# Kernel optimization log

Hardware: AMD Instinct MI355X
Metric: run time of the kernel (lower is better)

## Reference

```python
import jax, jax.numpy as jnp
import numpy as np

N = 100000   # num_nodes_total
E = 1600000  # num edges (avg degree 16)
ES = 30000   # scored triples
R = 16       # num_relations
D = 128      # cfg.dim


def setup_inputs() -> dict:
    key = jax.random.key(0)
    ks = jax.random.split(key, 10)
    x0 = 0.01 * jax.random.normal(ks[0], (N, D), dtype=jnp.float32)  # Embedding init std=0.01
    # GCNConv lin: Glorot init, no bias in lin; separate zero bias added post-aggregation
    glorot = np.sqrt(6.0 / (D + D)).astype(np.float32)
    W1 = jax.random.uniform(ks[1], (D, D), jnp.float32, -glorot, glorot)
    b1 = jnp.zeros((D,), jnp.float32)
    W2 = jax.random.uniform(ks[2], (D, D), jnp.float32, -glorot, glorot)
    b2 = jnp.zeros((D,), jnp.float32)
    rel_W = jax.random.uniform(ks[3], (R, D, D), jnp.float32, -glorot, glorot)  # xavier_uniform
    edge_index = jax.random.randint(ks[4], (2, E), 0, N)
    rel_ids = jax.random.randint(ks[5], (ES,), 0, R)
    head = jax.random.randint(ks[6], (ES,), 0, N)
    tail = jax.random.randint(ks[7], (ES,), 0, N)
    return {"x0": x0, "W1": W1, "b1": b1, "W2": W2, "b2": b2,
            "rel_W": rel_W, "edge_index": edge_index, "rel_ids": rel_ids,
            "head": head, "tail": tail}


def _gcn_conv(x, W, b, src, dst, norm):
    # GCNConv(add_self_loops=False, normalize=True): out = scatter(norm * (xW)[src] -> dst) + b
    h = x @ W                           # (N, D)
    msg = h[src] * norm[:, None]        # (E, D)
    return jax.ops.segment_sum(msg, dst, num_segments=x.shape[0]) + b


def reference(x0, W1, b1, W2, b2, rel_W, edge_index, rel_ids, head, tail):
    src, dst = edge_index[0], edge_index[1]
    n = x0.shape[0]
    # symmetric gcn_norm without self-loops: deg over targets, norm = d^-1/2[src]*d^-1/2[dst]
    deg = jax.ops.segment_sum(jnp.ones_like(src, dtype=x0.dtype), dst, num_segments=n)
    dinv = jnp.where(deg > 0, 1.0 / jnp.sqrt(jnp.maximum(deg, 1.0)), 0.0)
    norm = dinv[src] * dinv[dst]
    # encode (eval mode: dropout is identity)
    x = jax.nn.relu(_gcn_conv(x0, W1, b1, src, dst, norm))
    z = _gcn_conv(x, W2, b2, src, dst, norm)
    # score_logits_all_rel: z[head]^T W[rel] z[tail]
    scores = jnp.einsum('ed,edf,ef->e', z[head], rel_W[rel_ids], z[tail])
    return scores
```

## Files before the change

### kernel.cpp

```cpp
#include <hip/hip_runtime.h>
#include <hip/hip_bf16.h>

#define TD 128
#define WS 136
#define SC_T 8
#define BKT_SH 7
#define NBLK 256

typedef __attribute__((ext_vector_type(8))) short bf16x8;
typedef __attribute__((ext_vector_type(4))) float f32x4;

static __device__ __forceinline__ unsigned short f2bf(float f) {
    unsigned int u = __float_as_uint(f);
    u += 0x7fffu + ((u >> 16) & 1u);
    return (unsigned short)(u >> 16);
}
static __device__ __forceinline__ float bf2f(unsigned short h) {
    return __uint_as_float((unsigned int)h << 16);
}


__global__ __launch_bounds__(256) void kc_hist(const int* __restrict__ ei, int* __restrict__ bh,
                                               const int* __restrict__ rel, int* __restrict__ rcount,
                                               int E_, int ES_, int NB, int chunk, int rchunk) {
    __shared__ int lh[1024];
    __shared__ int rh[16];
    int t = threadIdx.x, blk = blockIdx.x;
    for (int j = t; j < NB; j += 256) lh[j] = 0;
    if (t < 16) rh[t] = 0;
    __syncthreads();
    int e0 = blk * chunk, e1 = min(E_, e0 + chunk);
    for (int e = e0 + t; e < e1; e += 256)
        atomicAdd(&lh[ei[E_ + e] >> BKT_SH], 1);
    int r0 = blk * rchunk, r1 = min(ES_, r0 + rchunk);
    for (int e = r0 + t; e < r1; e += 256)
        atomicAdd(&rh[rel[e]], 1);
    __syncthreads();
    for (int j = t; j < NB; j += 256) bh[(size_t)j * NBLK + blk] = lh[j];
    if (t < 16 && rh[t]) atomicAdd(&rcount[t], rh[t]);
}

__global__ __launch_bounds__(64) void kc_scanA(int* __restrict__ bh, int* __restrict__ tot, int NB) {
    int b = blockIdx.x, l = threadIdx.x;
    int* row = bh + (size_t)b * NBLK;
    int run = 0;
#pragma unroll
    for (int g = 0; g < NBLK / 64; ++g) {
        int v = row[g * 64 + l];
        int x = v;
#pragma unroll
        for (int off = 1; off < 64; off <<= 1) {
            int y = __shfl_up(x, off);
            if (l >= off) x += y;
        }
        row[g * 64 + l] = run + x - v;
        run += __shfl(x, 63);
    }
    if (l == 0) tot[b] = run;
}

__global__ __launch_bounds__(256) void kc_scanB(const int* __restrict__ tot, int* __restrict__ boff,
                                                int NB, int* __restrict__ rowptrN) {
    __shared__ int wsum[4];
    int t = threadIdx.x;
    int base = t * 4;
    int a0 = (base     < NB) ? tot[base]     : 0;
    int a1 = (base + 1 < NB) ? tot[base + 1] : 0;
    int a2 = (base + 2 < NB) ? tot[base + 2] : 0;
    int a3 = (base + 3 < NB) ? tot[base + 3] : 0;
    int s1 = a0 + a1, s2 = s1 + a2, tt = s2 + a3;
    int lane = t & 63, wv = t >> 6;
    int x = tt;
#pragma unroll
    for (int off = 1; off < 64; off <<= 1) {
        int y = __shfl_up(x, off);
        if (lane >= off) x += y;
    }
    if (lane == 63) wsum[wv] = x;
    __syncthreads();
    int woff = 0;
    for (int w = 0; w < wv; ++w) woff += wsum[w];
    int excl = woff + x - tt;
    if (base     < NB) boff[base]     = excl;
    if (base + 1 < NB) boff[base + 1] = excl + a0;
    if (base + 2 < NB) boff[base + 2] = excl + s1;
    if (base + 3 < NB) boff[base + 3] = excl + s2;
    if (t == 255) { boff[NB] = woff + x; *rowptrN = woff + x; }
}

__global__ __launch_bounds__(256) void kc_scat(const int* __restrict__ ei, const int* __restrict__ bh,
                                               const int* __restrict__ boff, int* __restrict__ ebuf,
                                               int E_, int NB, int chunk) {
    __shared__ int lh[1024];
    int t = threadIdx.x, blk = blockIdx.x;
    for (int j = t; j < NB; j += 256) lh[j] = 0;
    __syncthreads();
    int e0 = blk * chunk, e1 = min(E_, e0 + chunk);
    for (int e = e0 + t; e < e1; e += 256) {
        int s = ei[e];
        int d = ei[E_ + e];
        int b = d >> BKT_SH;
        int lr = atomicAdd(&lh[b], 1);
        int slot = boff[b] + bh[(size_t)b * NBLK + blk] + lr;
        ebuf[slot] = (s << BKT_SH) | (d & ((1 << BKT_SH) - 1));
    }
}

__global__ __launch_bounds__(256) void kc_build(const int* __restrict__ ebuf, const int* __restrict__ boff,
                                                int* __restrict__ rowptr, float* __restrict__ dinv,
                                                int* __restrict__ esrc, int n) {
    __shared__ int hist[128], excl[128], cur[128];
    __shared__ int w0;
    int b = blockIdx.x, t = threadIdx.x;
    int node0 = b << BKT_SH;
    int s = boff[b], e = boff[b + 1];
    if (t < 128) { hist[t] = 0; cur[t] = 0; }
    __syncthreads();
    for (int i = s + t; i < e; i += 256)
        atomicAdd(&hist[ebuf[i] & 127], 1);
    __syncthreads();
    int v = (t < 128) ? hist[t] : 0;
    int lane = t & 63, wv = t >> 6;
    int x = v;
#pragma unroll
    for (int off = 1; off < 64; off <<= 1) {
        int y = __shfl_up(x, off);
        if (lane >= off) x += y;
    }
    if (t == 63) w0 = x;
    __syncthreads();
    if (t < 128) {
        int ex = x - v + (wv == 1 ? w0 : 0);
        excl[t] = ex;
        int node = node0 + t;
        if (node < n) {
            rowptr[node] = s + ex;
            dinv[node] = (v > 0) ? 1.0f / sqrtf((float)v) : 0.0f;
        }
    }
    __syncthreads();
    for (int i = s + t; i < e; i += 256) {
        int p = ebuf[i];
        int loc = p & 127;
        int lr = atomicAdd(&cur[loc], 1);
        esrc[s + excl[loc] + lr] = p >> BKT_SH;
    }
}

__global__ __launch_bounds__(256) void k_wsplit(const float* __restrict__ W1, const float* __restrict__ W2,
                                                unsigned short* __restrict__ Wt) {
    int i = blockIdx.x * 256 + threadIdx.x;
    int w = i >> 14;
    int idx = i & 16383;
    int k = idx >> 7, n = idx & 127;
    float x = (w ? W2 : W1)[idx];
    unsigned short h = f2bf(x);
    unsigned short l = f2bf(x - bf2f(h));
    size_t base = (size_t)w * 32768;
    Wt[base + n * 128 + k] = h;
    Wt[base + 16384 + n * 128 + k] = l;
}

__global__ __launch_bounds__(256, 2) void k_gemm(const float* __restrict__ X,
                                                 const unsigned short* __restrict__ Wth,
                                                 const unsigned short* __restrict__ Wtl,
                                                 const float* __restrict__ scale,
                                                 unsigned char* __restrict__ out8,
                                                 float* __restrict__ scOut,
                                                 int nrows) {
    __shared__ __align__(16) unsigned short Wl[2][128 * WS];
    const int t = threadIdx.x;
    const int w = t >> 6;
    const int lane = t & 63;
    const int l15 = lane & 15;
    const int quad = lane >> 4;
    const int rbase = blockIdx.x * 64 + w * 16;
    const int arow = rbase + l15;
    const bool avalid = arow < nrows;

    float4 xa[4][2];
#pragma unroll
    for (int kc = 0; kc < 4; ++kc) {
        const float* src = X + (size_t)arow * TD + kc * 32 + quad * 8;
        xa[kc][0] = avalid ? *(const float4*)src       : make_float4(0.f, 0.f, 0.f, 0.f);
        xa[kc][1] = avalid ? *(const float4*)(src + 4) : make_float4(0.f, 0.f, 0.f, 0.f);
    }

    {
        const uint4* gh = (const uint4*)Wth;
        const uint4* gl = (const uint4*)Wtl;
#pragma unroll
        for (int it = 0; it < 8; ++it) {
            int idx = t + it * 256;
            int n = idx >> 4, kg = idx & 15;
            uint4 vh = gh[idx];
            uint4 vl = gl[idx];
            *(uint4*)&Wl[0][n * WS + kg * 8] = vh;
            *(uint4*)&Wl[1][n * WS + kg * 8] = vl;
        }
    }

    bf16x8 ah[4], al[4];
#pragma unroll
    for (int kc = 0; kc < 4; ++kc) {
#pragma unroll
        for (int j = 0; j < 8; ++j) {
            float v = (j < 4) ? ((const float*)&xa[kc][0])[j] : ((const float*)&xa[kc][1])[j - 4];
            unsigned short h = f2bf(v);
            ah[kc][j] = (short)h;
            al[kc][j] = (short)f2bf(v - bf2f(h));
        }
    }
    __syncthreads();

    f32x4 acc[8];
#pragma unroll
    for (int b = 0; b < 8; ++b) acc[b] = (f32x4){0.f, 0.f, 0.f, 0.f};

#pragma unroll
    for (int kc = 0; kc < 4; ++kc) {
        const int koff = kc * 32 + quad * 8;
#pragma unroll
        for (int b = 0; b < 8; ++b) {
            const int boff = (b * 16 + l15) * WS + koff;
            bf16x8 bh = *(const bf16x8*)&Wl[0][boff];
            bf16x8 bl = *(const bf16x8*)&Wl[1][boff];
            acc[b] = __builtin_amdgcn_mfma_f32_16x16x32_bf16(ah[kc], bh, acc[b], 0, 0, 0);
            acc[b] = __builtin_amdgcn_mfma_f32_16x16x32_bf16(al[kc], bh, acc[b], 0, 0, 0);
            acc[b] = __builtin_amdgcn_mfma_f32_16x16x32_bf16(ah[kc], bl, acc[b], 0, 0, 0);
        }
    }

    __syncthreads();

    {
        unsigned char* lds8 = (unsigned char*)&Wl[0][0];
        const int grow = rbase + quad * 4;
        float4 s4 = make_float4(0.f, 0.f, 0.f, 0.f);
        if (grow < nrows) s4 = *(const float4*)&scale[grow];
        float rm[4];
#pragma unroll
        for (int j = 0; j < 4; ++j) {
            float sj = ((const float*)&s4)[j];
            float mx = 0.f;
#pragma unroll
            for (int b = 0; b < 8; ++b) {
                acc[b][j] *= sj;
                mx = fmaxf(mx, fabsf(acc[b][j]));
            }
            rm[j] = mx;
        }
#pragma unroll
        for (int m_ = 1; m_ < 16; m_ <<= 1)
#pragma unroll
            for (int j = 0; j < 4; ++j) rm[j] = fmaxf(rm[j], __shfl_xor(rm[j], m_));
        float inv[4];
#pragma unroll
        for (int j = 0; j < 4; ++j) inv[j] = rm[j] > 0.f ? 127.f / rm[j] : 0.f;
#pragma unroll
        for (int j = 0; j < 4; ++j) {
            int lrow = w * 16 + quad * 4 + j;
#pragma unroll
            for (int b = 0; b < 8; ++b) {
                int q = (int)rintf(acc[b][j] * inv[j]);
                lds8[lrow * 128 + b * 16 + l15] = (unsigned char)(signed char)q;
            }
        }
        if (l15 == 0 && grow < nrows)
            *(float4*)&scOut[grow] = make_float4(rm[0] * (1.f / 127.f), rm[1] * (1.f / 127.f),
                                                 rm[2] * (1.f / 127.f), rm[3] * (1.f / 127.f));
    }
    __syncthreads();
    {
        const unsigned int* lds32 = (const unsigned int*)&Wl[0][0];
        unsigned int* g32 = (unsigned int*)out8;
#pragma unroll
        for (int k = 0; k < 8; ++k) {
            int idx = t + k * 256;
            int row = blockIdx.x * 64 + (idx >> 5);
            if (row < nrows) g32[(size_t)blockIdx.x * 2048 + idx] = lds32[idx];
        }
    }
}

#define ACCI8(p, u, s) \
    p##0 = fmaf(s, (float)(signed char)(u.x      ), p##0); \
    p##1 = fmaf(s, (float)(signed char)(u.x >>  8), p##1); \
    p##2 = fmaf(s, (float)(signed char)(u.x >> 16), p##2); \
    p##3 = fmaf(s, (float)(signed char)(u.x >> 24), p##3); \
    p##4 = fmaf(s, (float)(signed char)(u.y      ), p##4); \
    p##5 = fmaf(s, (float)(signed char)(u.y >>  8), p##5); \
    p##6 = fmaf(s, (float)(signed char)(u.y >> 16), p##6); \
    p##7 = fmaf(s, (float)(signed char)(u.y >> 24), p##7);

__global__ __launch_bounds__(256) void k_agg(const unsigned char* __restrict__ hs8, const float* __restrict__ sc,
                                             const int* __restrict__ rowptr, const int* __restrict__ esrc,
                                             const float* __restrict__ dinv, const float* __restrict__ bias,
                                             float* __restrict__ out, int n, int relu) {
    int node = blockIdx.x * 16 + (threadIdx.x >> 4);
    int lane = threadIdx.x & 15;
    if (node >= n) return;
    int s = rowptr[node], e = rowptr[node + 1];
    const uint2* h8 = (const uint2*)hs8;
    float a0 = 0.f, a1 = 0.f, a2 = 0.f, a3 = 0.f, a4 = 0.f, a5 = 0.f, a6 = 0.f, a7 = 0.f;
    float c0 = 0.f, c1 = 0.f, c2 = 0.f, c3 = 0.f, c4 = 0.f, c5 = 0.f, c6 = 0.f, c7 = 0.f;
    int i = s;
    for (; i + 4 <= e; i += 4) {
        int s0 = esrc[i], s1 = esrc[i + 1], s2 = esrc[i + 2], s3 = esrc[i + 3];
        uint2 u0 = h8[(size_t)s0 * 16 + lane];
        uint2 u1 = h8[(size_t)s1 * 16 + lane];
        uint2 u2 = h8[(size_t)s2 * 16 + lane];
        uint2 u3 = h8[(size_t)s3 * 16 + lane];
        float f0 = sc[s0], f1 = sc[s1], f2 = sc[s2], f3 = sc[s3];
        ACCI8(a, u0, f0)
        ACCI8(c, u1, f1)
        ACCI8(a, u2, f2)
        ACCI8(c, u3, f3)
    }
    for (; i < e; ++i) {
        int s0 = esrc[i];
        uint2 u = h8[(size_t)s0 * 16 + lane];
        float f = sc[s0];
        ACCI8(a, u, f)
    }
    a0 += c0; a1 += c1; a2 += c2; a3 += c3;
    a4 += c4; a5 += c5; a6 += c6; a7 += c7;
    float di = dinv[node];
    float4 b0 = ((const float4*)bias)[lane * 2];
    float4 b1 = ((const float4*)bias)[lane * 2 + 1];
    float o0 = fmaf(di, a0, b0.x);
    float o1 = fmaf(di, a1, b0.y);
    float o2 = fmaf(di, a2, b0.z);
    float o3 = fmaf(di, a3, b0.w);
    float o4 = fmaf(di, a4, b1.x);
    float o5 = fmaf(di, a5, b1.y);
    float o6 = fmaf(di, a6, b1.z);
    float o7 = fmaf(di, a7, b1.w);
    if (relu) {
        o0 = fmaxf(o0, 0.f); o1 = fmaxf(o1, 0.f); o2 = fmaxf(o2, 0.f); o3 = fmaxf(o3, 0.f);
        o4 = fmaxf(o4, 0.f); o5 = fmaxf(o5, 0.f); o6 = fmaxf(o6, 0.f); o7 = fmaxf(o7, 0.f);
    }
    ((float4*)out)[(size_t)node * 32 + lane * 2]     = make_float4(o0, o1, o2, o3);
    ((float4*)out)[(size_t)node * 32 + lane * 2 + 1] = make_float4(o4, o5, o6, o7);
}

__global__ void k_roff(const int* __restrict__ rcount, int* __restrict__ roff,
                       int* __restrict__ chunkoff, int* __restrict__ cursor, int nr) {
    if (threadIdx.x == 0 && blockIdx.x == 0) {
        int run = 0, crun = 0;
        for (int r = 0; r < nr; ++r) {
            roff[r] = run; chunkoff[r] = crun; cursor[r] = run;
            run += rcount[r]; crun += (rcount[r] + SC_T - 1) / SC_T;
        }
        roff[nr] = run; chunkoff[nr] = crun;
    }
}

__global__ __launch_bounds__(256) void k_bucket(const int* __restrict__ rel, int* __restrict__ cursor,
                                                int* __restrict__ eidx, int es) {
    __shared__ int lh[16];
    __shared__ int lbase[16];
    int t = threadIdx.x;
    if (t < 16) lh[t] = 0;
    __syncthreads();
    int r[4], lr[4];
#pragma unroll
    for (int i = 0; i < 4; ++i) {
        int e = blockIdx.x * 1024 + i * 256 + t;
        if (e < es) {
            r[i] = rel[e];
            lr[i] = atomicAdd(&lh[r[i]], 1);
        } else r[i] = -1;
    }
    __syncthreads();
    if (t < 16) lbase[t] = lh[t] ? atomicAdd(&cursor[t], lh[t]) : 0;
    __syncthreads();
#pragma unroll
    for (int i = 0; i < 4; ++i)
        if (r[i] >= 0) eidx[lbase[r[i]] + lr[i]] = blockIdx.x * 1024 + i * 256 + t;
}

__global__ __launch_bounds__(256) void k_score_r(const float* __restrict__ z, const float* __restrict__ relW,
                                                 const int* __restrict__ eidx, const int* __restrict__ head,
                                                 const int* __restrict__ tail, const int* __restrict__ roff,
                                                 const int* __restrict__ chunkoff, float* __restrict__ out,
                                                 int R_, int cpb) {
    __shared__ __align__(16) float Wl[TD * TD];
    __shared__ __align__(16) float zhL[SC_T * TD];
    __shared__ __align__(16) float ztL[SC_T * TD];
    __shared__ int eids[SC_T];
    __shared__ int co[17], ro[17];
    __shared__ float red[4][SC_T];
    const int t = threadIdx.x;
    if (t < 17 && t <= R_) { co[t] = chunkoff[t]; ro[t] = roff[t]; }
    __syncthreads();
    const int nch = co[R_];
    int b = blockIdx.x * cpb;
    const int bend = min(nch, b + cpb);
    int r = 0, rprev = -1;
    for (; b < bend; ++b) {
        while (co[r + 1] <= b) ++r;
        const int base = ro[r] + (b - co[r]) * SC_T;
        const int nt = min(SC_T, ro[r + 1] - base);
        if (t < SC_T) eids[t] = (t < nt) ? eidx[base + t] : -1;
        const bool newW = (r != rprev);
        rprev = r;
        __syncthreads();
        {
            int tt = t >> 5, c4 = t & 31;
            float4 vh = make_float4(0.f, 0.f, 0.f, 0.f), vt = vh;
            int e = eids[tt];
            if (e >= 0) {
                vh = ((const float4*)(z + (size_t)head[e] * TD))[c4];
                vt = ((const float4*)(z + (size_t)tail[e] * TD))[c4];
            }
            ((float4*)(zhL + tt * TD))[c4] = vh;
            ((float4*)(ztL + tt * TD))[c4] = vt;
        }
        if (newW) {
            const float4* W4 = (const float4*)(relW + (size_t)r * TD * TD);
            float4* Wl4 = (float4*)Wl;
#pragma unroll
            for (int i = 0; i < 16; ++i) Wl4[t + i * 256] = W4[t + i * 256];
        }
        __syncthreads();

        const int c  = (t & 31) * 4;
        const int i0 = (t >> 5) * 16;
        float4 acc[SC_T];
#pragma unroll
        for (int u = 0; u < SC_T; ++u) acc[u] = make_float4(0.f, 0.f, 0.f, 0.f);
#pragma unroll 4
        for (int i = i0; i < i0 + 16; ++i) {
            float4 wv = *(const float4*)&Wl[i * TD + c];
#pragma unroll
            for (int u = 0; u < SC_T; ++u) {
                float h = zhL[u * TD + i];
                acc[u].x = fmaf(h, wv.x, acc[u].x);
                acc[u].y = fmaf(h, wv.y, acc[u].y);
                acc[u].z = fmaf(h, wv.z, acc[u].z);
                acc[u].w = fmaf(h, wv.w, acc[u].w);
            }
        }
        float pth[SC_T];
#pragma unroll
        for (int u = 0; u < SC_T; ++u) {
            float4 z4 = *(const float4*)&ztL[u * TD + c];
            pth[u] = acc[u].x * z4.x + acc[u].y * z4.y + acc[u].z * z4.z + acc[u].w * z4.w;
        }
#pragma unroll
        for (int off = 32; off > 0; off >>= 1)
#pragma unroll
            for (int u = 0; u < SC_T; ++u) pth[u] += __shfl_down(pth[u], off);
        if ((t & 63) == 0) {
            int wv = t >> 6;
#pragma unroll
            for (int u = 0; u < SC_T; ++u) red[wv][u] = pth[u];
        }
        __syncthreads();
        if (t < SC_T) {
            int e = eids[t];
            if (e >= 0) out[e] = red[0][t] + red[1][t] + red[2][t] + red[3][t];
        }
    }
}

extern "C" void kernel_launch(void* const* d_in, const int* in_sizes, int n_in,
                              void* d_out, int out_size, void* d_ws, size_t ws_size,
                              hipStream_t stream) {
    const float* x0   = (const float*)d_in[0];
    const float* W1   = (const float*)d_in[1];
    const float* b1   = (const float*)d_in[2];
    const float* W2   = (const float*)d_in[3];
    const float* b2   = (const float*)d_in[4];
    const float* relW = (const float*)d_in[5];
    const int*   ei   = (const int*)d_in[6];
    const int*   rel  = (const int*)d_in[7];
    const int*   head = (const int*)d_in[8];
    const int*   tail = (const int*)d_in[9];
    float* outp = (float*)d_out;

    const int N_  = in_sizes[0] / TD;
    const int E_  = in_sizes[6] / 2;
    const int ES_ = in_sizes[7];
    const int R_  = in_sizes[5] / (TD * TD);
    const int ntiles64 = (N_ + 63) / 64;
    const int NB    = (N_ + (1 << BKT_SH) - 1) >> BKT_SH;
    const int chunk  = (E_ + NBLK - 1) / NBLK;
    const int rchunk = (ES_ + NBLK - 1) / NBLK;
    const int maxch  = (ES_ + SC_T - 1) / SC_T + R_;
    const int sgrid  = maxch < 512 ? maxch : 512;
    const int cpb    = (maxch + sgrid - 1) / sgrid;

    char* p = (char*)d_ws;
    auto alloc = [&](size_t bytes) { char* r = p; p += (bytes + 255) & ~(size_t)255; return r; };
    float*          dinv   = (float*)         alloc((size_t)N_ * 4);
    int*            rowptr = (int*)           alloc(((size_t)N_ + 1) * 4);
    int*            bh     = (int*)           alloc((size_t)NB * NBLK * 4);
    int*            tot    = (int*)           alloc((size_t)NB * 4);
    int*            boff   = (int*)           alloc(((size_t)NB + 1) * 4);
    int*            esrc   = (int*)           alloc((size_t)E_ * 4);
    unsigned short* Wt     = (unsigned short*)alloc((size_t)4 * 16384 * 2);
    int*            rcount = (int*)           alloc((size_t)R_ * 4);
    int*            roff   = (int*)           alloc(((size_t)R_ + 1) * 4);
    int*            chkoff = (int*)           alloc(((size_t)R_ + 1) * 4);
    int*            cursor = (int*)           alloc((size_t)R_ * 4);
    int*            eidx   = (int*)           alloc((size_t)ES_ * 4);
    unsigned char*  bufA   = (unsigned char*) alloc((size_t)N_ * TD);
    float*          sc     = (float*)         alloc((size_t)N_ * 4);
    float*          bufB   = (float*)         alloc((size_t)N_ * TD * 4);
    int*            ebuf   = (int*)bufA;

    hipMemsetAsync(rcount, 0, (size_t)R_ * 4, stream);

    kc_hist <<<NBLK, 256, 0, stream>>>(ei, bh, rel, rcount, E_, ES_, NB, chunk, rchunk);
    kc_scanA<<<NB, 64, 0, stream>>>(bh, tot, NB);
    kc_scanB<<<1, 256, 0, stream>>>(tot, boff, NB, rowptr + N_);
    kc_scat <<<NBLK, 256, 0, stream>>>(ei, bh, boff, ebuf, E_, NB, chunk);
    kc_build<<<NB, 256, 0, stream>>>(ebuf, boff, rowptr, dinv, esrc, N_);

    k_wsplit<<<128, 256, 0, stream>>>(W1, W2, Wt);

    k_roff  <<<1, 64, 0, stream>>>(rcount, roff, chkoff, cursor, R_);
    k_bucket<<<(ES_ + 1023) / 1024, 256, 0, stream>>>(rel, cursor, eidx, ES_);

    k_gemm<<<ntiles64, 256, 0, stream>>>(x0, Wt, Wt + 16384, dinv, bufA, sc, N_);
    k_agg <<<(N_ + 15) / 16, 256, 0, stream>>>(bufA, sc, rowptr, esrc, dinv, b1, bufB, N_, 1);
    k_gemm<<<ntiles64, 256, 0, stream>>>(bufB, Wt + 32768, Wt + 49152, dinv, bufA, sc, N_);
    k_agg <<<(N_ + 15) / 16, 256, 0, stream>>>(bufA, sc, rowptr, esrc, dinv, b2, bufB, N_, 0);

    k_score_r<<<sgrid, 256, 0, stream>>>(bufB, relW, eidx, head, tail,
                                         roff, chkoff, outp, R_, cpb);
}
```

Baseline: 326.1 us.

## Drop split-bf16 GEMM to single bf16 and fuse small setup kernels

The GCN GEMM moves from a three-MFMA split-bf16 emulation of fp32 (hi*hi, lo*hi, hi*lo) to a single bf16 MFMA. This halves the weight LDS footprint, so launch bounds rise to four blocks per SM. The weight conversion moves into extra blocks of the histogram kernel, and the relation-offset computation folds into the scan kernel, which removes two launches. The cost is accuracy: the inputs and weights are now plain bf16, which may loosen agreement with the fp32 reference.

```diff
diff --git a/kernel.cpp b/kernel.cpp
--- a/kernel.cpp
+++ b/kernel.cpp
@@ -22,10 +22,19 @@
 
 __global__ __launch_bounds__(256) void kc_hist(const int* __restrict__ ei, int* __restrict__ bh,
                                                const int* __restrict__ rel, int* __restrict__ rcount,
+                                               const float* __restrict__ W1, const float* __restrict__ W2,
+                                               unsigned short* __restrict__ Wt,
                                                int E_, int ES_, int NB, int chunk, int rchunk) {
     __shared__ int lh[1024];
     __shared__ int rh[16];
     int t = threadIdx.x, blk = blockIdx.x;
+    if (blk >= NBLK) {
+        int idx = (blk - NBLK) * 256 + t;
+        int k = idx >> 7, n = idx & 127;
+        Wt[n * 128 + k] = f2bf(W1[idx]);
+        Wt[16384 + n * 128 + k] = f2bf(W2[idx]);
+        return;
+    }
     for (int j = t; j < NB; j += 256) lh[j] = 0;
     if (t < 16) rh[t] = 0;
     __syncthreads();
@@ -60,7 +69,9 @@
 }
 
 __global__ __launch_bounds__(256) void kc_scanB(const int* __restrict__ tot, int* __restrict__ boff,
-                                                int NB, int* __restrict__ rowptrN) {
+                                                int NB, int* __restrict__ rowptrN,
+                                                const int* __restrict__ rcount, int* __restrict__ roff,
+                                                int* __restrict__ chunkoff, int* __restrict__ cursor, int nr) {
     __shared__ int wsum[4];
     int t = threadIdx.x;
     int base = t * 4;
@@ -86,6 +97,14 @@
     if (base + 2 < NB) boff[base + 2] = excl + s1;
     if (base + 3 < NB) boff[base + 3] = excl + s2;
     if (t == 255) { boff[NB] = woff + x; *rowptrN = woff + x; }
+    if (t == 0) {
+        int run = 0, crun = 0;
+        for (int r = 0; r < nr; ++r) {
+            roff[r] = run; chunkoff[r] = crun; cursor[r] = run;
+            run += rcount[r]; crun += (rcount[r] + SC_T - 1) / SC_T;
+        }
+        roff[nr] = run; chunkoff[nr] = crun;
+    }
 }
 
 __global__ __launch_bounds__(256) void kc_scat(const int* __restrict__ ei, const int* __restrict__ bh,
@@ -147,28 +166,13 @@
     }
 }
 
-__global__ __launch_bounds__(256) void k_wsplit(const float* __restrict__ W1, const float* __restrict__ W2,
-                                                unsigned short* __restrict__ Wt) {
-    int i = blockIdx.x * 256 + threadIdx.x;
-    int w = i >> 14;
-    int idx = i & 16383;
-    int k = idx >> 7, n = idx & 127;
-    float x = (w ? W2 : W1)[idx];
-    unsigned short h = f2bf(x);
-    unsigned short l = f2bf(x - bf2f(h));
-    size_t base = (size_t)w * 32768;
-    Wt[base + n * 128 + k] = h;
-    Wt[base + 16384 + n * 128 + k] = l;
-}
-
-__global__ __launch_bounds__(256, 2) void k_gemm(const float* __restrict__ X,
+__global__ __launch_bounds__(256, 4) void k_gemm(const float* __restrict__ X,
                                                  const unsigned short* __restrict__ Wth,
-                                                 const unsigned short* __restrict__ Wtl,
                                                  const float* __restrict__ scale,
                                                  unsigned char* __restrict__ out8,
                                                  float* __restrict__ scOut,
                                                  int nrows) {
-    __shared__ __align__(16) unsigned short Wl[2][128 * WS];
+    __shared__ __align__(16) unsigned short Wl[128 * WS];
     const int t = threadIdx.x;
     const int w = t >> 6;
     const int lane = t & 63;
@@ -188,27 +192,22 @@
 
     {
         const uint4* gh = (const uint4*)Wth;
-        const uint4* gl = (const uint4*)Wtl;
 #pragma unroll
         for (int it = 0; it < 8; ++it) {
             int idx = t + it * 256;
             int n = idx >> 4, kg = idx & 15;
             uint4 vh = gh[idx];
-            uint4 vl = gl[idx];
-            *(uint4*)&Wl[0][n * WS + kg * 8] = vh;
-            *(uint4*)&Wl[1][n * WS + kg * 8] = vl;
-        }
-    }
-
-    bf16x8 ah[4], al[4];
+            *(uint4*)&Wl[n * WS + kg * 8] = vh;
+        }
+    }
+
+    bf16x8 ah[4];
 #pragma unroll
     for (int kc = 0; kc < 4; ++kc) {
 #pragma unroll
         for (int j = 0; j < 8; ++j) {
             float v = (j < 4) ? ((const float*)&xa[kc][0])[j] : ((const float*)&xa[kc][1])[j - 4];
-            unsigned short h = f2bf(v);
-            ah[kc][j] = (short)h;
-            al[kc][j] = (short)f2bf(v - bf2f(h));
+            ah[kc][j] = (short)f2bf(v);
         }
     }
     __syncthreads();
@@ -222,19 +221,15 @@
         const int koff = kc * 32 + quad * 8;
 #pragma unroll
         for (int b = 0; b < 8; ++b) {
-            const int boff = (b * 16 + l15) * WS + koff;
-            bf16x8 bh = *(const bf16x8*)&Wl[0][boff];
-            bf16x8 bl = *(const bf16x8*)&Wl[1][boff];
+            bf16x8 bh = *(const bf16x8*)&Wl[(b * 16 + l15) * WS + koff];
             acc[b] = __builtin_amdgcn_mfma_f32_16x16x32_bf16(ah[kc], bh, acc[b], 0, 0, 0);
-            acc[b] = __builtin_amdgcn_mfma_f32_16x16x32_bf16(al[kc], bh, acc[b], 0, 0, 0);
-            acc[b] = __builtin_amdgcn_mfma_f32_16x16x32_bf16(ah[kc], bl, acc[b], 0, 0, 0);
         }
     }
 
     __syncthreads();
 
     {
-        unsigned char* lds8 = (unsigned char*)&Wl[0][0];
+        unsigned char* lds8 = (unsigned char*)&Wl[0];
         const int grow = rbase + quad * 4;
         float4 s4 = make_float4(0.f, 0.f, 0.f, 0.f);
         if (grow < nrows) s4 = *(const float4*)&scale[grow];
@@ -272,7 +267,7 @@
     }
     __syncthreads();
     {
-        const unsigned int* lds32 = (const unsigned int*)&Wl[0][0];
+        const unsigned int* lds32 = (const unsigned int*)&Wl[0];
         unsigned int* g32 = (unsigned int*)out8;
 #pragma unroll
         for (int k = 0; k < 8; ++k) {
@@ -344,18 +339,6 @@
     ((float4*)out)[(size_t)node * 32 + lane * 2 + 1] = make_float4(o4, o5, o6, o7);
 }
 
-__global__ void k_roff(const int* __restrict__ rcount, int* __restrict__ roff,
-                       int* __restrict__ chunkoff, int* __restrict__ cursor, int nr) {
-    if (threadIdx.x == 0 && blockIdx.x == 0) {
-        int run = 0, crun = 0;
-        for (int r = 0; r < nr; ++r) {
-            roff[r] = run; chunkoff[r] = crun; cursor[r] = run;
-            run += rcount[r]; crun += (rcount[r] + SC_T - 1) / SC_T;
-        }
-        roff[nr] = run; chunkoff[nr] = crun;
-    }
-}
-
 __global__ __launch_bounds__(256) void k_bucket(const int* __restrict__ rel, int* __restrict__ cursor,
                                                 int* __restrict__ eidx, int es) {
     __shared__ int lh[16];
@@ -500,7 +483,7 @@
     int*            tot    = (int*)           alloc((size_t)NB * 4);
     int*            boff   = (int*)           alloc(((size_t)NB + 1) * 4);
     int*            esrc   = (int*)           alloc((size_t)E_ * 4);
-    unsigned short* Wt     = (unsigned short*)alloc((size_t)4 * 16384 * 2);
+    unsigned short* Wt     = (unsigned short*)alloc((size_t)2 * 16384 * 2);
     int*            rcount = (int*)           alloc((size_t)R_ * 4);
     int*            roff   = (int*)           alloc(((size_t)R_ + 1) * 4);
     int*            chkoff = (int*)           alloc(((size_t)R_ + 1) * 4);
@@ -513,20 +496,17 @@
 
     hipMemsetAsync(rcount, 0, (size_t)R_ * 4, stream);
 
-    kc_hist <<<NBLK, 256, 0, stream>>>(ei, bh, rel, rcount, E_, ES_, NB, chunk, rchunk);
+    kc_hist <<<NBLK + 64, 256, 0, stream>>>(ei, bh, rel, rcount, W1, W2, Wt, E_, ES_, NB, chunk, rchunk);
     kc_scanA<<<NB, 64, 0, stream>>>(bh, tot, NB);
-    kc_scanB<<<1, 256, 0, stream>>>(tot, boff, NB, rowptr + N_);
+    kc_scanB<<<1, 256, 0, stream>>>(tot, boff, NB, rowptr + N_, rcount, roff, chkoff, cursor, R_);
     kc_scat <<<NBLK, 256, 0, stream>>>(ei, bh, boff, ebuf, E_, NB, chunk);
     kc_build<<<NB, 256, 0, stream>>>(ebuf, boff, rowptr, dinv, esrc, N_);
 
-    k_wsplit<<<128, 256, 0, stream>>>(W1, W2, Wt);
-
-    k_roff  <<<1, 64, 0, stream>>>(rcount, roff, chkoff, cursor, R_);
     k_bucket<<<(ES_ + 1023) / 1024, 256, 0, stream>>>(rel, cursor, eidx, ES_);
 
-    k_gemm<<<ntiles64, 256, 0, stream>>>(x0, Wt, Wt + 16384, dinv, bufA, sc, N_);
+    k_gemm<<<ntiles64, 256, 0, stream>>>(x0, Wt, dinv, bufA, sc, N_);
     k_agg <<<(N_ + 15) / 16, 256, 0, stream>>>(bufA, sc, rowptr, esrc, dinv, b1, bufB, N_, 1);
-    k_gemm<<<ntiles64, 256, 0, stream>>>(bufB, Wt + 32768, Wt + 49152, dinv, bufA, sc, N_);
+    k_gemm<<<ntiles64, 256, 0, stream>>>(bufB, Wt + 16384, dinv, bufA, sc, N_);
     k_agg <<<(N_ + 15) / 16, 256, 0, stream>>>(bufA, sc, rowptr, esrc, dinv, b2, bufB, N_, 0);
 
     k_score_r<<<sgrid, 256, 0, stream>>>(bufB, relW, eidx, head, tail,
```

After: 305.3 us. 1.07x faster.
